# Performance work log

Measured on AMD Instinct MI355X. Metric: run time of the kernel, lower is better.

Reference implementation:

```python
import jax, jax.numpy as jnp
import numpy as np

N_NODES = 100000
N_EDGES = 1600000
IN_CH = 128
HID_CH = 128


def setup_inputs() -> dict:
    key = jax.random.key(0)
    ks = jax.random.split(key, 10)
    x = jax.random.normal(ks[0], (N_NODES, IN_CH), dtype=jnp.float32)
    edge_index = jax.random.randint(ks[1], (2, N_EDGES), 0, N_NODES, dtype=jnp.int64)
    s1 = 1.0 / np.sqrt(IN_CH)
    s2 = 1.0 / np.sqrt(HID_CH)
    return {
        "x": x,
        "edge_index": edge_index,
        "W1": jax.random.uniform(ks[2], (IN_CH, HID_CH), jnp.float32, -s1, s1),
        "b1": jnp.zeros((HID_CH,), jnp.float32),
        "W2": jax.random.uniform(ks[3], (HID_CH, HID_CH), jnp.float32, -s2, s2),
        "b2": jnp.zeros((HID_CH,), jnp.float32),
        "We": jax.random.uniform(ks[4], (IN_CH, HID_CH), jnp.float32, -s1, s1),
        "be": jax.random.uniform(ks[5], (HID_CH,), jnp.float32, -s1, s1),
        "Wfc": jax.random.uniform(ks[6], (HID_CH, 1), jnp.float32, -s2, s2),
        "bfc": jax.random.uniform(ks[7], (1,), jnp.float32, -s2, s2),
    }


def _gcn_conv(x, src, dst, norm, W, b, n_nodes):
    # PyG GCNConv: linear transform, then normalized scatter-add aggregation, then bias
    h = x @ W                                 # [N, H]
    msg = h[src] * norm[:, None]              # gather + scale  [E+N, H]
    out = jax.ops.segment_sum(msg, dst, num_segments=n_nodes)  # scatter-add [N, H]
    return out + b


def reference(x, edge_index, W1, b1, W2, b2, We, be, Wfc, bfc):
    n = x.shape[0]
    # add self-loops (PyG default add_self_loops=True)
    loop = jnp.arange(n, dtype=edge_index.dtype)
    src = jnp.concatenate([edge_index[0], loop])
    dst = jnp.concatenate([edge_index[1], loop])
    # symmetric degree normalization deg^-1/2 (edge_weight implicitly ones)
    deg = jax.ops.segment_sum(jnp.ones_like(src, dtype=x.dtype), dst, num_segments=n)
    dinv = jnp.where(deg > 0, jax.lax.rsqrt(deg), 0.0)
    norm = dinv[src] * dinv[dst]

    x_conv = jax.nn.relu(_gcn_conv(x, src, dst, norm, W1, b1, n))
    x_fc = jax.nn.relu(x @ We + be)
    h = x_conv + x_fc                          # residual; dropout is identity in eval
    x_conv2 = jax.nn.relu(_gcn_conv(h, src, dst, norm, W2, b2, n))
    h = x_conv2 + h
    # batch is all zeros -> global_mean_pool == mean over all nodes -> [1, H]
    pooled = jnp.mean(h, axis=0, keepdims=True)
    predict = jax.nn.sigmoid(pooled @ Wfc + bfc)  # [1, 1]
    return predict
```

## Files before the change

### kernel.cpp

```cpp
#include <hip/hip_runtime.h>
#include <hip/hip_bf16.h>

typedef unsigned int uint;
typedef unsigned short ushort;
typedef unsigned char uchar;
typedef __attribute__((ext_vector_type(8))) short short8;
typedef __attribute__((ext_vector_type(4))) float f32x4;
typedef __attribute__((ext_vector_type(4))) uint u32x4;

__device__ __forceinline__ float bf2f(ushort u) {
    union { uint i; float f; } v; v.i = ((uint)u) << 16; return v.f;
}
__device__ __forceinline__ ushort f2bf(float f) {
    union { float f; uint i; } v; v.f = f;
    uint x = v.i;
    uint r = (x + 0x7FFFu + ((x >> 16) & 1u)) >> 16;
    return (ushort)r;
}
__device__ __forceinline__ uchar f2q(float f) {
    return (uchar)(__builtin_amdgcn_cvt_pk_fp8_f32(f, 0.f, 0, false) & 0xFF);
}
__device__ __forceinline__ void q2f4(uint w, float* o) {
    o[0] = __builtin_amdgcn_cvt_f32_fp8(w, 0);
    o[1] = __builtin_amdgcn_cvt_f32_fp8(w, 1);
    o[2] = __builtin_amdgcn_cvt_f32_fp8(w, 2);
    o[3] = __builtin_amdgcn_cvt_f32_fp8(w, 3);
}


__global__ void k_degree(const int* __restrict__ dst, int* __restrict__ deg,
                         int e, int n) {
    int bin = blockIdx.x & 7;
    int sub = blockIdx.x >> 3;
    int nsub = gridDim.x >> 3;
    int q = (n + 7) >> 3;
    int lo = bin * q, hi = min(n, lo + q);
    for (int i = sub * 256 + threadIdx.x; i < e; i += nsub * 256) {
        int d = dst[i];
        if (d >= lo && d < hi) atomicAdd(&deg[d], 1);
    }
}

__global__ void k_dinv(const int* __restrict__ deg, float* __restrict__ dinv, int n) {
    int i = blockIdx.x * 256 + threadIdx.x;
    if (i < n) dinv[i] = rsqrtf((float)deg[i] + 1.0f);
}

__global__ void k_scan_a(const int* __restrict__ deg, int* __restrict__ bsum, int n) {
    __shared__ int sd[256];
    int t = threadIdx.x;
    int base = blockIdx.x * 1024 + t * 4;
    int s = 0;
#pragma unroll
    for (int j = 0; j < 4; ++j) { int idx = base + j; if (idx < n) s += deg[idx]; }
    sd[t] = s; __syncthreads();
    for (int off = 1; off < 256; off <<= 1) {
        int v = (t >= off) ? sd[t - off] : 0;
        __syncthreads();
        sd[t] += v;
        __syncthreads();
    }
    if (t == 255) bsum[blockIdx.x] = sd[255];
}

__global__ void k_scan_b(const int* __restrict__ bsum, int* __restrict__ boff, int nb) {
    __shared__ int sd[256];
    int t = threadIdx.x;
    int v0 = (t < nb) ? bsum[t] : 0;
    sd[t] = v0; __syncthreads();
    for (int off = 1; off < 256; off <<= 1) {
        int v = (t >= off) ? sd[t - off] : 0;
        __syncthreads();
        sd[t] += v;
        __syncthreads();
    }
    if (t < nb) boff[t] = sd[t] - v0;
}

__global__ void k_scan_c(const int* __restrict__ deg, const int* __restrict__ boff,
                         int* __restrict__ offs, int n) {
    __shared__ int sd[256];
    int t = threadIdx.x;
    int base = blockIdx.x * 1024 + t * 4;
    int vals[4]; int s = 0;
#pragma unroll
    for (int j = 0; j < 4; ++j) {
        int idx = base + j;
        vals[j] = (idx < n) ? deg[idx] : 0;
        s += vals[j];
    }
    sd[t] = s; __syncthreads();
    for (int off = 1; off < 256; off <<= 1) {
        int v = (t >= off) ? sd[t - off] : 0;
        __syncthreads();
        sd[t] += v;
        __syncthreads();
    }
    int run = boff[blockIdx.x] + (sd[t] - s);
#pragma unroll
    for (int j = 0; j < 4; ++j) {
        int idx = base + j;
        if (idx < n) { offs[idx] = run; run += vals[j]; }
    }
}

__global__ void k_fill(const int* __restrict__ src, const int* __restrict__ dst,
                       const int* __restrict__ offs, int* __restrict__ cursor,
                       int* __restrict__ csr, int e, int n) {
    int bin = blockIdx.x & 7;
    int sub = blockIdx.x >> 3;
    int nsub = gridDim.x >> 3;
    int q = (n + 7) >> 3;
    int lo = bin * q, hi = min(n, lo + q);
    for (int i = sub * 256 + threadIdx.x; i < e; i += nsub * 256) {
        int d = dst[i];
        if (d >= lo && d < hi) {
            int p = offs[d] + atomicAdd(&cursor[d], 1);
            csr[p] = src[i];
        }
    }
}


__global__ __launch_bounds__(512) void k_gemm1(
    const float* __restrict__ x, const float* __restrict__ W1, const float* __restrict__ We,
    const float* __restrict__ be, const float* __restrict__ dinv,
    uchar* __restrict__ h1q, ushort* __restrict__ xfc, int n)
{
    __shared__ __align__(16) ushort Bt[256][72];
    int tid = threadIdx.x;
    int w = tid >> 6, lane = tid & 63;
    int ln15 = lane & 15, g = lane >> 4;
    int rowBase = blockIdx.x * 128 + w * 16;
    int r = rowBase + ln15;
    bool valid = r < n;
    size_t slice = (size_t)(n + 1) * 32;

    short8 a[4];
#pragma unroll
    for (int ks = 0; ks < 4; ++ks) {
        float4 f0 = make_float4(0.f, 0.f, 0.f, 0.f), f1 = f0;
        if (valid) {
            const float* p = x + (size_t)r * 128 + ks * 32 + g * 8;
            f0 = *reinterpret_cast<const float4*>(p);
            f1 = *reinterpret_cast<const float4*>(p + 4);
        }
        short8 v;
        v[0] = (short)f2bf(f0.x); v[1] = (short)f2bf(f0.y);
        v[2] = (short)f2bf(f0.z); v[3] = (short)f2bf(f0.w);
        v[4] = (short)f2bf(f1.x); v[5] = (short)f2bf(f1.y);
        v[6] = (short)f2bf(f1.z); v[7] = (short)f2bf(f1.w);
        a[ks] = v;
    }

    f32x4 acc[16];
#pragma unroll
    for (int i = 0; i < 16; ++i) acc[i] = (f32x4){0.f, 0.f, 0.f, 0.f};

    for (int s = 0; s < 2; ++s) {
        for (int i = tid; i < 8192; i += 512) {
            int kl = i >> 7, j = i & 127;
            int kg = s * 64 + kl;
            Bt[j][kl]       = f2bf(W1[kg * 128 + j]);
            Bt[128 + j][kl] = f2bf(We[kg * 128 + j]);
        }
        __syncthreads();
#pragma unroll
        for (int t2 = 0; t2 < 2; ++t2) {
            short8 af = a[s * 2 + t2];
#pragma unroll
            for (int jf = 0; jf < 16; ++jf) {
                short8 bf = *reinterpret_cast<const short8*>(&Bt[jf * 16 + ln15][t2 * 32 + g * 8]);
                acc[jf] = __builtin_amdgcn_mfma_f32_16x16x32_bf16(af, bf, acc[jf], 0, 0, 0);
            }
        }
        __syncthreads();
    }

    float dv[4];
#pragma unroll
    for (int q = 0; q < 4; ++q) {
        int rr = rowBase + g * 4 + q;
        dv[q] = (rr < n) ? dinv[rr] : 0.f;
    }

#pragma unroll
    for (int jf = 0; jf < 16; ++jf) {
        int col = jf * 16 + ln15;
#pragma unroll
        for (int q = 0; q < 4; ++q) {
            int rr = rowBase + g * 4 + q;
            if (rr < n) {
                float v = acc[jf][q];
                if (col < 128) {
                    h1q[(size_t)(col >> 5) * slice + (size_t)rr * 32 + (col & 31)] = f2q(v * dv[q]);
                } else {
                    float vv = fmaxf(v + be[col - 128], 0.f);
                    xfc[(size_t)rr * 128 + (col - 128)] = f2bf(vv);
                }
            }
        }
    }
}


__global__ __launch_bounds__(512) void k_gemm2(
    const ushort* __restrict__ h, const float* __restrict__ W2, const float* __restrict__ dinv,
    uchar* __restrict__ h2q, int n)
{
    __shared__ __align__(16) ushort Bt[128][72];
    int tid = threadIdx.x;
    int w = tid >> 6, lane = tid & 63;
    int ln15 = lane & 15, g = lane >> 4;
    int rowBase = blockIdx.x * 128 + w * 16;
    int r = rowBase + ln15;
    bool valid = r < n;
    size_t slice = (size_t)(n + 1) * 32;

    short8 a[4];
#pragma unroll
    for (int ks = 0; ks < 4; ++ks) {
        short8 v = (short8){0,0,0,0,0,0,0,0};
        if (valid) v = *reinterpret_cast<const short8*>(h + (size_t)r * 128 + ks * 32 + g * 8);
        a[ks] = v;
    }

    f32x4 acc[8];
#pragma unroll
    for (int i = 0; i < 8; ++i) acc[i] = (f32x4){0.f, 0.f, 0.f, 0.f};

    for (int s = 0; s < 2; ++s) {
        for (int i = tid; i < 8192; i += 512) {
            int kl = i >> 7, j = i & 127;
            Bt[j][kl] = f2bf(W2[(s * 64 + kl) * 128 + j]);
        }
        __syncthreads();
#pragma unroll
        for (int t2 = 0; t2 < 2; ++t2) {
            short8 af = a[s * 2 + t2];
#pragma unroll
            for (int jf = 0; jf < 8; ++jf) {
                short8 bf = *reinterpret_cast<const short8*>(&Bt[jf * 16 + ln15][t2 * 32 + g * 8]);
                acc[jf] = __builtin_amdgcn_mfma_f32_16x16x32_bf16(af, bf, acc[jf], 0, 0, 0);
            }
        }
        __syncthreads();
    }

    float dv[4];
#pragma unroll
    for (int q = 0; q < 4; ++q) {
        int rr = rowBase + g * 4 + q;
        dv[q] = (rr < n) ? dinv[rr] : 0.f;
    }

#pragma unroll
    for (int jf = 0; jf < 8; ++jf) {
        int col = jf * 16 + ln15;
#pragma unroll
        for (int q = 0; q < 4; ++q) {
            int rr = rowBase + g * 4 + q;
            if (rr < n)
                h2q[(size_t)(col >> 5) * slice + (size_t)rr * 32 + (col & 31)] = f2q(acc[jf][q] * dv[q]);
        }
    }
}


__global__ __launch_bounds__(256) void k_agg1(
    const int* __restrict__ csr, const int* __restrict__ offs, const int* __restrict__ degE,
    const float* __restrict__ dinv, const uchar* __restrict__ h1q, const ushort* __restrict__ xfc,
    const float* __restrict__ b1, ushort* __restrict__ h, int n, int nodeBlocks)
{
    int t = threadIdx.x;
    int chunk = blockIdx.x / nodeBlocks;
    int nb = blockIdx.x - chunk * nodeBlocks;
    int pair = t >> 1, sub = t & 1;
    int node = nb * 128 + pair;
    if (node >= n) return;
    size_t slice = (size_t)(n + 1) * 32;
    const uchar* tbl = h1q + (size_t)chunk * slice + sub * 16;
    int off = offs[node], cnt = degE[node];
    float di = dinv[node];
    float acc[16];
#pragma unroll
    for (int e = 0; e < 16; ++e) acc[e] = 0.f;

    for (int base = 0; base < cnt; base += 8) {
        u32x4 u[8];
#pragma unroll
        for (int q = 0; q < 8; ++q) {
            int s = __builtin_nontemporal_load(csr + off + base + q);
            int id = (base + q < cnt) ? s : n;
            u[q] = *reinterpret_cast<const u32x4*>(tbl + (size_t)id * 32);
        }
#pragma unroll
        for (int q = 0; q < 8; ++q) {
            float d4[4];
            q2f4(u[q][0], d4); acc[0] += d4[0]; acc[1] += d4[1]; acc[2] += d4[2]; acc[3] += d4[3];
            q2f4(u[q][1], d4); acc[4] += d4[0]; acc[5] += d4[1]; acc[6] += d4[2]; acc[7] += d4[3];
            q2f4(u[q][2], d4); acc[8] += d4[0]; acc[9] += d4[1]; acc[10] += d4[2]; acc[11] += d4[3];
            q2f4(u[q][3], d4); acc[12] += d4[0]; acc[13] += d4[1]; acc[14] += d4[2]; acc[15] += d4[3];
        }
    }

    u32x4 us = *reinterpret_cast<const u32x4*>(tbl + (size_t)node * 32);
    float sdec[16];
    q2f4(us[0], sdec); q2f4(us[1], sdec + 4); q2f4(us[2], sdec + 8); q2f4(us[3], sdec + 12);
    int c0 = chunk * 32 + sub * 16;
    const u32x4* xp = reinterpret_cast<const u32x4*>(xfc + (size_t)node * 128 + c0);
    u32x4 x0 = __builtin_nontemporal_load(xp);
    u32x4 x1 = __builtin_nontemporal_load(xp + 1);
    uint xw[8] = {x0[0], x0[1], x0[2], x0[3], x1[0], x1[1], x1[2], x1[3]};
    float bb[16];
#pragma unroll
    for (int p = 0; p < 4; ++p) {
        float4 bq = *reinterpret_cast<const float4*>(b1 + c0 + p * 4);
        bb[4 * p] = bq.x; bb[4 * p + 1] = bq.y; bb[4 * p + 2] = bq.z; bb[4 * p + 3] = bq.w;
    }
    uint outw[8];
#pragma unroll
    for (int j = 0; j < 8; ++j) {
        int e0 = 2 * j, e1 = 2 * j + 1;
        float v0 = fmaxf((acc[e0] + sdec[e0]) * di + bb[e0], 0.f) + bf2f((ushort)(xw[j] & 0xffff));
        float v1 = fmaxf((acc[e1] + sdec[e1]) * di + bb[e1], 0.f) + bf2f((ushort)(xw[j] >> 16));
        outw[j] = (uint)f2bf(v0) | ((uint)f2bf(v1) << 16);
    }
    ushort* hp = h + (size_t)node * 128 + c0;
    u32x4 o0 = {outw[0], outw[1], outw[2], outw[3]};
    u32x4 o1 = {outw[4], outw[5], outw[6], outw[7]};
    __builtin_nontemporal_store(o0, reinterpret_cast<u32x4*>(hp));
    __builtin_nontemporal_store(o1, reinterpret_cast<u32x4*>(hp + 8));
}


__global__ __launch_bounds__(256) void k_agg2(
    const int* __restrict__ csr, const int* __restrict__ offs, const int* __restrict__ degE,
    const float* __restrict__ dinv, const uchar* __restrict__ h2q, const ushort* __restrict__ hres,
    const float* __restrict__ b2, float* __restrict__ pooled, int n, int nodeBlocks)
{
    __shared__ float lpool[128];
    int t = threadIdx.x;
    if (t < 128) lpool[t] = 0.f;
    __syncthreads();
    int chunk = blockIdx.x / nodeBlocks;
    int nb = blockIdx.x - chunk * nodeBlocks;
    int pair = t >> 1, sub = t & 1;
    int node = nb * 128 + pair;
    bool valid = node < n;
    int nodeC = valid ? node : (n - 1);
    size_t slice = (size_t)(n + 1) * 32;
    const uchar* tbl = h2q + (size_t)chunk * slice + sub * 16;
    int off = offs[nodeC];
    int cnt = valid ? degE[nodeC] : 0;
    float di = dinv[nodeC];
    float acc[16];
#pragma unroll
    for (int e = 0; e < 16; ++e) acc[e] = 0.f;

    for (int base = 0; base < cnt; base += 8) {
        u32x4 u[8];
#pragma unroll
        for (int q = 0; q < 8; ++q) {
            int s = __builtin_nontemporal_load(csr + off + base + q);
            int id = (base + q < cnt) ? s : n;
            u[q] = *reinterpret_cast<const u32x4*>(tbl + (size_t)id * 32);
        }
#pragma unroll
        for (int q = 0; q < 8; ++q) {
            float d4[4];
            q2f4(u[q][0], d4); acc[0] += d4[0]; acc[1] += d4[1]; acc[2] += d4[2]; acc[3] += d4[3];
            q2f4(u[q][1], d4); acc[4] += d4[0]; acc[5] += d4[1]; acc[6] += d4[2]; acc[7] += d4[3];
            q2f4(u[q][2], d4); acc[8] += d4[0]; acc[9] += d4[1]; acc[10] += d4[2]; acc[11] += d4[3];
            q2f4(u[q][3], d4); acc[12] += d4[0]; acc[13] += d4[1]; acc[14] += d4[2]; acc[15] += d4[3];
        }
    }

    u32x4 us = *reinterpret_cast<const u32x4*>(tbl + (size_t)nodeC * 32);
    float sdec[16];
    q2f4(us[0], sdec); q2f4(us[1], sdec + 4); q2f4(us[2], sdec + 8); q2f4(us[3], sdec + 12);
    int c0 = chunk * 32 + sub * 16;
    const u32x4* rp = reinterpret_cast<const u32x4*>(hres + (size_t)nodeC * 128 + c0);
    u32x4 r0 = __builtin_nontemporal_load(rp);
    u32x4 r1 = __builtin_nontemporal_load(rp + 1);
    uint rw[8] = {r0[0], r0[1], r0[2], r0[3], r1[0], r1[1], r1[2], r1[3]};
    float bb[16];
#pragma unroll
    for (int p = 0; p < 4; ++p) {
        float4 bq = *reinterpret_cast<const float4*>(b2 + c0 + p * 4);
        bb[4 * p] = bq.x; bb[4 * p + 1] = bq.y; bb[4 * p + 2] = bq.z; bb[4 * p + 3] = bq.w;
    }
    if (valid) {
#pragma unroll
        for (int j = 0; j < 8; ++j) {
            int e0 = 2 * j, e1 = 2 * j + 1;
            float v0 = fmaxf((acc[e0] + sdec[e0]) * di + bb[e0], 0.f) + bf2f((ushort)(rw[j] & 0xffff));
            float v1 = fmaxf((acc[e1] + sdec[e1]) * di + bb[e1], 0.f) + bf2f((ushort)(rw[j] >> 16));
            atomicAdd(&lpool[c0 + e0], v0);
            atomicAdd(&lpool[c0 + e1], v1);
        }
    }
    __syncthreads();
    if (t < 32) atomicAdd(&pooled[chunk * 32 + t], lpool[chunk * 32 + t]);
}


__global__ void k_final(const float* __restrict__ pooled, const float* __restrict__ Wfc,
                        const float* __restrict__ bfc, float* __restrict__ out, float invN) {
    int lane = threadIdx.x;
    float s = pooled[2 * lane] * invN * Wfc[2 * lane] +
              pooled[2 * lane + 1] * invN * Wfc[2 * lane + 1];
#pragma unroll
    for (int off = 32; off > 0; off >>= 1) s += __shfl_down(s, off);
    if (lane == 0) out[0] = 1.f / (1.f + expf(-(s + bfc[0])));
}


extern "C" void kernel_launch(void* const* d_in, const int* in_sizes, int n_in,
                              void* d_out, int out_size, void* d_ws, size_t ws_size,
                              hipStream_t stream) {
    const float* x   = (const float*)d_in[0];
    const int*   ei  = (const int*)d_in[1];
    const float* W1  = (const float*)d_in[2];
    const float* b1  = (const float*)d_in[3];
    const float* W2  = (const float*)d_in[4];
    const float* b2  = (const float*)d_in[5];
    const float* We  = (const float*)d_in[6];
    const float* be  = (const float*)d_in[7];
    const float* Wfc = (const float*)d_in[8];
    const float* bfc = (const float*)d_in[9];
    float* out = (float*)d_out;

    const int N = in_sizes[0] / 128;
    const int E = in_sizes[1] / 2;
    const int* src = ei;
    const int* dst = ei + E;

    char* w = (char*)d_ws;
    size_t off = 0;
    auto take = [&](size_t bytes) -> void* {
        void* p = w + off;
        off = (off + bytes + 255) & ~(size_t)255;
        return p;
    };
    int*    deg    = (int*)take((size_t)N * 4);
    int*    offs   = (int*)take((size_t)N * 4);
    int*    cursor = (int*)take((size_t)N * 4);
    float*  dinv   = (float*)take((size_t)N * 4);
    int*    bsum   = (int*)take(1024);
    int*    boff   = (int*)take(1024);
    int*    csr    = (int*)take((size_t)(E + 64) * 4);
    uchar*  h1q    = (uchar*)take((size_t)(N + 1) * 128);
    ushort* xfc    = (ushort*)take((size_t)N * 128 * 2);
    ushort* h      = (ushort*)take((size_t)N * 128 * 2);
    uchar*  h2q    = (uchar*)take((size_t)(N + 1) * 128);
    float*  pooled = (float*)take(512);

    const size_t slice = (size_t)(N + 1) * 32;
    const int nbScan = (N + 1023) / 1024;
    const int nodeBlocks = (N + 127) / 128;

    hipMemsetAsync(deg, 0, (size_t)N * 4, stream);
    hipMemsetAsync(cursor, 0, (size_t)N * 4, stream);
    hipMemsetAsync(pooled, 0, 512, stream);
    for (int p = 0; p < 4; ++p) {
        hipMemsetAsync(h1q + p * slice + (size_t)N * 32, 0, 32, stream);
        hipMemsetAsync(h2q + p * slice + (size_t)N * 32, 0, 32, stream);
    }

    k_degree<<<2048, 256, 0, stream>>>(dst, deg, E, N);
    k_dinv<<<(N + 255) / 256, 256, 0, stream>>>(deg, dinv, N);
    k_scan_a<<<nbScan, 256, 0, stream>>>(deg, bsum, N);
    k_scan_b<<<1, 256, 0, stream>>>(bsum, boff, nbScan);
    k_scan_c<<<nbScan, 256, 0, stream>>>(deg, boff, offs, N);
    k_fill<<<2048, 256, 0, stream>>>(src, dst, offs, cursor, csr, E, N);

    k_gemm1<<<(N + 127) / 128, 512, 0, stream>>>(x, W1, We, be, dinv, h1q, xfc, N);
    k_agg1<<<4 * nodeBlocks, 256, 0, stream>>>(csr, offs, deg, dinv, h1q, xfc, b1, h, N, nodeBlocks);
    k_gemm2<<<(N + 127) / 128, 512, 0, stream>>>(h, W2, dinv, h2q, N);
    k_agg2<<<4 * nodeBlocks, 256, 0, stream>>>(csr, offs, deg, dinv, h2q, h, b2, pooled, N, nodeBlocks);
    k_final<<<1, 64, 0, stream>>>(pooled, Wfc, bfc, out, 1.0f / (float)N);
}
```

Before: 448.0 us.

## Store fp8 features row-major and aggregate full rows with 8 threads per node

The fp8 feature tables move from four column-chunked slices to a plain row-major [N+1,128] layout. The aggregation kernels now assign 8 threads per node covering all 128 channels, instead of 2 threads per node for one of 4 chunk passes. Each edge then gathers a full 128-byte row in one pass, and CSR indices are read once rather than four times, with 16 edges batched per loop. Nontemporal hints are dropped. The risks are more registers from the 16-deep gather buffers and lower occupancy.

```diff
diff --git a/kernel.cpp b/kernel.cpp
--- a/kernel.cpp
+++ b/kernel.cpp
@@ -134,7 +134,6 @@
     int rowBase = blockIdx.x * 128 + w * 16;
     int r = rowBase + ln15;
     bool valid = r < n;
-    size_t slice = (size_t)(n + 1) * 32;
 
     short8 a[4];
 #pragma unroll
@@ -193,7 +192,7 @@
             if (rr < n) {
                 float v = acc[jf][q];
                 if (col < 128) {
-                    h1q[(size_t)(col >> 5) * slice + (size_t)rr * 32 + (col & 31)] = f2q(v * dv[q]);
+                    h1q[(size_t)rr * 128 + col] = f2q(v * dv[q]);
                 } else {
                     float vv = fmaxf(v + be[col - 128], 0.f);
                     xfc[(size_t)rr * 128 + (col - 128)] = f2bf(vv);
@@ -215,7 +214,6 @@
     int rowBase = blockIdx.x * 128 + w * 16;
     int r = rowBase + ln15;
     bool valid = r < n;
-    size_t slice = (size_t)(n + 1) * 32;
 
     short8 a[4];
 #pragma unroll
@@ -260,8 +258,7 @@
 #pragma unroll
         for (int q = 0; q < 4; ++q) {
             int rr = rowBase + g * 4 + q;
-            if (rr < n)
-                h2q[(size_t)(col >> 5) * slice + (size_t)rr * 32 + (col & 31)] = f2q(acc[jf][q] * dv[q]);
+            if (rr < n) h2q[(size_t)rr * 128 + col] = f2q(acc[jf][q] * dv[q]);
         }
     }
 }
@@ -270,32 +267,33 @@
 __global__ __launch_bounds__(256) void k_agg1(
     const int* __restrict__ csr, const int* __restrict__ offs, const int* __restrict__ degE,
     const float* __restrict__ dinv, const uchar* __restrict__ h1q, const ushort* __restrict__ xfc,
-    const float* __restrict__ b1, ushort* __restrict__ h, int n, int nodeBlocks)
+    const float* __restrict__ b1, ushort* __restrict__ h, int n)
 {
     int t = threadIdx.x;
-    int chunk = blockIdx.x / nodeBlocks;
-    int nb = blockIdx.x - chunk * nodeBlocks;
-    int pair = t >> 1, sub = t & 1;
-    int node = nb * 128 + pair;
+    int g = t >> 3, li = t & 7;
+    int node = blockIdx.x * 32 + g;
     if (node >= n) return;
-    size_t slice = (size_t)(n + 1) * 32;
-    const uchar* tbl = h1q + (size_t)chunk * slice + sub * 16;
     int off = offs[node], cnt = degE[node];
     float di = dinv[node];
+    int c0 = li * 16;
+    const uchar* tbl = h1q + c0;
     float acc[16];
 #pragma unroll
     for (int e = 0; e < 16; ++e) acc[e] = 0.f;
 
-    for (int base = 0; base < cnt; base += 8) {
-        u32x4 u[8];
-#pragma unroll
-        for (int q = 0; q < 8; ++q) {
-            int s = __builtin_nontemporal_load(csr + off + base + q);
-            int id = (base + q < cnt) ? s : n;
-            u[q] = *reinterpret_cast<const u32x4*>(tbl + (size_t)id * 32);
-        }
-#pragma unroll
-        for (int q = 0; q < 8; ++q) {
+    for (int base = 0; base < cnt; base += 16) {
+        int idx[16];
+#pragma unroll
+        for (int q = 0; q < 16; ++q) {
+            int s = csr[off + base + q];
+            idx[q] = (base + q < cnt) ? s : n;
+        }
+        u32x4 u[16];
+#pragma unroll
+        for (int q = 0; q < 16; ++q)
+            u[q] = *reinterpret_cast<const u32x4*>(tbl + (size_t)idx[q] * 128);
+#pragma unroll
+        for (int q = 0; q < 16; ++q) {
             float d4[4];
             q2f4(u[q][0], d4); acc[0] += d4[0]; acc[1] += d4[1]; acc[2] += d4[2]; acc[3] += d4[3];
             q2f4(u[q][1], d4); acc[4] += d4[0]; acc[5] += d4[1]; acc[6] += d4[2]; acc[7] += d4[3];
@@ -304,13 +302,11 @@
         }
     }
 
-    u32x4 us = *reinterpret_cast<const u32x4*>(tbl + (size_t)node * 32);
+    u32x4 us = *reinterpret_cast<const u32x4*>(tbl + (size_t)node * 128);
     float sdec[16];
     q2f4(us[0], sdec); q2f4(us[1], sdec + 4); q2f4(us[2], sdec + 8); q2f4(us[3], sdec + 12);
-    int c0 = chunk * 32 + sub * 16;
     const u32x4* xp = reinterpret_cast<const u32x4*>(xfc + (size_t)node * 128 + c0);
-    u32x4 x0 = __builtin_nontemporal_load(xp);
-    u32x4 x1 = __builtin_nontemporal_load(xp + 1);
+    u32x4 x0 = xp[0], x1 = xp[1];
     uint xw[8] = {x0[0], x0[1], x0[2], x0[3], x1[0], x1[1], x1[2], x1[3]};
     float bb[16];
 #pragma unroll
@@ -329,45 +325,46 @@
     ushort* hp = h + (size_t)node * 128 + c0;
     u32x4 o0 = {outw[0], outw[1], outw[2], outw[3]};
     u32x4 o1 = {outw[4], outw[5], outw[6], outw[7]};
-    __builtin_nontemporal_store(o0, reinterpret_cast<u32x4*>(hp));
-    __builtin_nontemporal_store(o1, reinterpret_cast<u32x4*>(hp + 8));
+    *reinterpret_cast<u32x4*>(hp) = o0;
+    *reinterpret_cast<u32x4*>(hp + 8) = o1;
 }
 
 
 __global__ __launch_bounds__(256) void k_agg2(
     const int* __restrict__ csr, const int* __restrict__ offs, const int* __restrict__ degE,
     const float* __restrict__ dinv, const uchar* __restrict__ h2q, const ushort* __restrict__ hres,
-    const float* __restrict__ b2, float* __restrict__ pooled, int n, int nodeBlocks)
+    const float* __restrict__ b2, float* __restrict__ pooled, int n)
 {
     __shared__ float lpool[128];
     int t = threadIdx.x;
     if (t < 128) lpool[t] = 0.f;
     __syncthreads();
-    int chunk = blockIdx.x / nodeBlocks;
-    int nb = blockIdx.x - chunk * nodeBlocks;
-    int pair = t >> 1, sub = t & 1;
-    int node = nb * 128 + pair;
+    int g = t >> 3, li = t & 7;
+    int node = blockIdx.x * 32 + g;
     bool valid = node < n;
     int nodeC = valid ? node : (n - 1);
-    size_t slice = (size_t)(n + 1) * 32;
-    const uchar* tbl = h2q + (size_t)chunk * slice + sub * 16;
     int off = offs[nodeC];
     int cnt = valid ? degE[nodeC] : 0;
     float di = dinv[nodeC];
+    int c0 = li * 16;
+    const uchar* tbl = h2q + c0;
     float acc[16];
 #pragma unroll
     for (int e = 0; e < 16; ++e) acc[e] = 0.f;
 
-    for (int base = 0; base < cnt; base += 8) {
-        u32x4 u[8];
-#pragma unroll
-        for (int q = 0; q < 8; ++q) {
-            int s = __builtin_nontemporal_load(csr + off + base + q);
-            int id = (base + q < cnt) ? s : n;
-            u[q] = *reinterpret_cast<const u32x4*>(tbl + (size_t)id * 32);
-        }
-#pragma unroll
-        for (int q = 0; q < 8; ++q) {
+    for (int base = 0; base < cnt; base += 16) {
+        int idx[16];
+#pragma unroll
+        for (int q = 0; q < 16; ++q) {
+            int s = csr[off + base + q];
+            idx[q] = (base + q < cnt) ? s : n;
+        }
+        u32x4 u[16];
+#pragma unroll
+        for (int q = 0; q < 16; ++q)
+            u[q] = *reinterpret_cast<const u32x4*>(tbl + (size_t)idx[q] * 128);
+#pragma unroll
+        for (int q = 0; q < 16; ++q) {
             float d4[4];
             q2f4(u[q][0], d4); acc[0] += d4[0]; acc[1] += d4[1]; acc[2] += d4[2]; acc[3] += d4[3];
             q2f4(u[q][1], d4); acc[4] += d4[0]; acc[5] += d4[1]; acc[6] += d4[2]; acc[7] += d4[3];
@@ -376,13 +373,11 @@
         }
     }
 
-    u32x4 us = *reinterpret_cast<const u32x4*>(tbl + (size_t)nodeC * 32);
+    u32x4 us = *reinterpret_cast<const u32x4*>(tbl + (size_t)nodeC * 128);
     float sdec[16];
     q2f4(us[0], sdec); q2f4(us[1], sdec + 4); q2f4(us[2], sdec + 8); q2f4(us[3], sdec + 12);
-    int c0 = chunk * 32 + sub * 16;
     const u32x4* rp = reinterpret_cast<const u32x4*>(hres + (size_t)nodeC * 128 + c0);
-    u32x4 r0 = __builtin_nontemporal_load(rp);
-    u32x4 r1 = __builtin_nontemporal_load(rp + 1);
+    u32x4 r0 = rp[0], r1 = rp[1];
     uint rw[8] = {r0[0], r0[1], r0[2], r0[3], r1[0], r1[1], r1[2], r1[3]};
     float bb[16];
 #pragma unroll
@@ -401,7 +396,7 @@
         }
     }
     __syncthreads();
-    if (t < 32) atomicAdd(&pooled[chunk * 32 + t], lpool[chunk * 32 + t]);
+    if (t < 128) atomicAdd(&pooled[t], lpool[t]);
 }
 
 
@@ -456,17 +451,13 @@
     uchar*  h2q    = (uchar*)take((size_t)(N + 1) * 128);
     float*  pooled = (float*)take(512);
 
-    const size_t slice = (size_t)(N + 1) * 32;
     const int nbScan = (N + 1023) / 1024;
-    const int nodeBlocks = (N + 127) / 128;
 
     hipMemsetAsync(deg, 0, (size_t)N * 4, stream);
     hipMemsetAsync(cursor, 0, (size_t)N * 4, stream);
     hipMemsetAsync(pooled, 0, 512, stream);
-    for (int p = 0; p < 4; ++p) {
-        hipMemsetAsync(h1q + p * slice + (size_t)N * 32, 0, 32, stream);
-        hipMemsetAsync(h2q + p * slice + (size_t)N * 32, 0, 32, stream);
-    }
+    hipMemsetAsync(h1q + (size_t)N * 128, 0, 128, stream);
+    hipMemsetAsync(h2q + (size_t)N * 128, 0, 128, stream);
 
     k_degree<<<2048, 256, 0, stream>>>(dst, deg, E, N);
     k_dinv<<<(N + 255) / 256, 256, 0, stream>>>(deg, dinv, N);
@@ -476,8 +467,8 @@
     k_fill<<<2048, 256, 0, stream>>>(src, dst, offs, cursor, csr, E, N);
 
     k_gemm1<<<(N + 127) / 128, 512, 0, stream>>>(x, W1, We, be, dinv, h1q, xfc, N);
-    k_agg1<<<4 * nodeBlocks, 256, 0, stream>>>(csr, offs, deg, dinv, h1q, xfc, b1, h, N, nodeBlocks);
+    k_agg1<<<(N + 31) / 32, 256, 0, stream>>>(csr, offs, deg, dinv, h1q, xfc, b1, h, N);
     k_gemm2<<<(N + 127) / 128, 512, 0, stream>>>(h, W2, dinv, h2q, N);
-    k_agg2<<<4 * nodeBlocks, 256, 0, stream>>>(csr, offs, deg, dinv, h2q, h, b2, pooled, N, nodeBlocks);
+    k_agg2<<<(N + 31) / 32, 256, 0, stream>>>(csr, offs, deg, dinv, h2q, h, b2, pooled, N);
     k_final<<<1, 64, 0, stream>>>(pooled, Wfc, bfc, out, 1.0f / (float)N);
 }
```

New measurement: 423.6 us. -5.5%, faster.
